# Kernel optimization log

Hardware: AMD Instinct MI355X
Metric: run time of the kernel (lower is better)

## Reference

```python
import jax, jax.numpy as jnp
import numpy as np

T, N, H, L, V, B, MAX_NB = 32, 1024, 256, 128, 800, 256, 15
E = T * N  # total messages; buffer row E is the zero-pad slot


def setup_inputs() -> dict:
    key = jax.random.key(0)
    ks = jax.random.split(key, 12)

    def lin(k, o, i):
        return jax.random.normal(k, (o, i), jnp.float32) / np.float32(np.sqrt(i))

    rng = np.random.default_rng(0)
    # neighbor message indices: at step t only messages produced at steps < t are valid
    h_nei_idx = rng.integers(0, E, size=(T, N, MAX_NB))
    o_nei_idx = rng.integers(0, E, size=(T, N, MAX_NB))
    limit = (np.arange(T) * N)[:, None, None]
    h_nei_idx = np.where(h_nei_idx < limit, h_nei_idx, E)
    o_nei_idx = np.where(o_nei_idx < limit, o_nei_idx, E)

    return dict(
        emb=jax.random.normal(ks[0], (V, H), jnp.float32) * 0.02,
        W_z_w=lin(ks[1], H, 2 * H), W_z_b=jnp.zeros((H,), jnp.float32),
        W_r_w=lin(ks[2], H, H), W_r_b=jnp.zeros((H,), jnp.float32),
        U_r_w=lin(ks[3], H, H),
        W_h_w=lin(ks[4], H, 2 * H), W_h_b=jnp.zeros((H,), jnp.float32),
        W_w=lin(ks[5], H, H + L), W_b=jnp.zeros((H,), jnp.float32),
        Wo_w=lin(ks[6], V, H), Wo_b=jnp.zeros((V,), jnp.float32),
        U_w=lin(ks[7], H, H + L), U_b=jnp.zeros((H,), jnp.float32),
        Ui_w=lin(ks[8], H, 2 * H), Ui_b=jnp.zeros((H,), jnp.float32),
        Uo_w=lin(ks[9], 1, H), Uo_b=jnp.zeros((1,), jnp.float32),
        x_tree_vecs=jax.random.normal(ks[10], (B, L), jnp.float32),
        word_ids=jnp.asarray(rng.integers(0, V, size=(T, N)), jnp.int32),
        h_nei_idx=jnp.asarray(h_nei_idx, jnp.int32),
        o_nei_idx=jnp.asarray(o_nei_idx, jnp.int32),
        contexts=jnp.asarray(rng.integers(0, B, size=(T, N)), jnp.int32),
        pred_targets=jnp.asarray(rng.integers(0, V, size=(T, N)), jnp.int32),
        direction=jnp.asarray(rng.integers(0, 2, size=(T, N)), jnp.int32),
        root_word_ids=jnp.asarray(rng.integers(0, V, size=(B,)), jnp.int32),
        root_o_idx=jnp.asarray(rng.integers(0, E + 1, size=(B, MAX_NB)), jnp.int32),
    )


def reference(emb, W_z_w, W_z_b, W_r_w, W_r_b, U_r_w, W_h_w, W_h_b,
              W_w, W_b, Wo_w, Wo_b, U_w, U_b, Ui_w, Ui_b, Uo_w, Uo_b,
              x_tree_vecs, word_ids, h_nei_idx, o_nei_idx, contexts,
              pred_targets, direction, root_word_ids, root_o_idx):
    f32 = jnp.float32

    def gru(x, h_nei):  # x: [N,H], h_nei: [N,MAX_NB,H]
        sum_h = h_nei.sum(1)
        z = jax.nn.sigmoid(jnp.concatenate([x, sum_h], -1) @ W_z_w.T + W_z_b)
        r = jax.nn.sigmoid((x @ W_r_w.T + W_r_b)[:, None, :] + h_nei @ U_r_w.T)
        gated = (r * h_nei).sum(1)
        h_tilde = jnp.tanh(jnp.concatenate([x, gated], -1) @ W_h_w.T + W_h_b)
        return (1.0 - z) * sum_h + z * h_tilde

    def step(hbuf, xs):
        t, wid, hidx, oidx = xs
        x = emb[wid]                      # [N,H] embedding gather
        new_h = gru(x, hbuf[hidx])        # gather -> GRU
        cur_o = hbuf[oidx].sum(1)         # padded neighbor sum for stop head
        hbuf = jax.lax.dynamic_update_slice(hbuf, new_h, (t * N, 0))  # scatter
        return hbuf, (new_h, jnp.concatenate([x, cur_o], -1))

    hbuf0 = jnp.zeros((E + 1, H), f32)
    hbuf, (new_h_all, stop_h_all) = jax.lax.scan(
        step, hbuf0, (jnp.arange(T), word_ids, h_nei_idx, o_nei_idx))

    def aggregate(hid, ctx, Vw, Vb, Vow, Vob):
        iv = jnp.concatenate([hid, x_tree_vecs[ctx]], -1)
        return jax.nn.relu(iv @ Vw.T + Vb) @ Vow.T + Vob

    # ---- word prediction head: root entries (zero hidden) + direction==1 edges
    pred_hid = jnp.concatenate([jnp.zeros((B, H), f32), new_h_all.reshape(E, H)], 0)
    pred_ctx = jnp.concatenate([jnp.arange(B, dtype=jnp.int32), contexts.reshape(E)], 0)
    pred_tgt = jnp.concatenate([root_word_ids, pred_targets.reshape(E)], 0)
    pred_mask = jnp.concatenate([jnp.ones((B,), f32), direction.reshape(E).astype(f32)], 0)
    scores = aggregate(pred_hid, pred_ctx, W_w, W_b, Wo_w, Wo_b)  # [B+E, V]
    nll = -jnp.take_along_axis(jax.nn.log_softmax(scores, -1), pred_tgt[:, None], 1)[:, 0]
    pred_loss = (nll * pred_mask).sum() / B
    pred_acc = ((scores.argmax(-1) == pred_tgt).astype(f32) * pred_mask).sum() / pred_mask.sum()

    # ---- stop head: all edges + root closing entries
    root_stop = jnp.concatenate([emb[root_word_ids], hbuf[root_o_idx].sum(1)], -1)
    stop_hid = jnp.concatenate([stop_h_all.reshape(E, 2 * H), root_stop], 0)
    stop_ctx = jnp.concatenate([contexts.reshape(E), jnp.arange(B, dtype=jnp.int32)], 0)
    stop_tgt = jnp.concatenate([direction.reshape(E).astype(f32), jnp.zeros((B,), f32)], 0)
    stop_hid = jax.nn.relu(stop_hid @ Ui_w.T + Ui_b)  # U_i with relu
    s = aggregate(stop_hid, stop_ctx, U_w, U_b, Uo_w, Uo_b)[:, 0]
    bce = jnp.maximum(s, 0.0) - s * stop_tgt + jnp.log1p(jnp.exp(-jnp.abs(s)))
    stop_loss = bce.sum() / B
    stop_acc = ((s >= 0.0).astype(f32) == stop_tgt).astype(f32).mean()

    return pred_loss, stop_loss, pred_acc, stop_acc
```

## Files before the change

kernel.cpp:

```cpp
#include <hip/hip_runtime.h>
#include <math.h>


namespace {

constexpr int T_  = 32;
constexpr int N_  = 1024;
constexpr int H_  = 256;
constexpr int NB_ = 15;
constexpr int E_  = T_ * N_;
constexpr int B_  = 256;
constexpr int PREDB_ = (B_ + E_) / 64;
constexpr int STOPB_ = (E_ + B_) / 64;

typedef unsigned short u16;
typedef unsigned int   u32;
typedef unsigned int  uix4  __attribute__((ext_vector_type(4)));
typedef __bf16        bf16x8 __attribute__((ext_vector_type(8)));
typedef float         f32x4  __attribute__((ext_vector_type(4)));

__device__ __forceinline__ float sig_(float x){ return 1.f / (1.f + __expf(-x)); }

__device__ __forceinline__ float b2f(u16 u){
  union { u32 i; float f; } v; v.i = ((u32)u) << 16; return v.f;
}
__device__ __forceinline__ u16 f2b(float f){
  union { float f; u32 i; } v; v.f = f;
  const u32 r = v.i + 0x7fffu + ((v.i >> 16) & 1u);
  return (u16)(r >> 16);
}
__device__ __forceinline__ f32x4 mfma16(uix4 a, uix4 b, f32x4 c){
  return __builtin_amdgcn_mfma_f32_16x16x32_bf16(
      __builtin_bit_cast(bf16x8, a), __builtin_bit_cast(bf16x8, b), c, 0, 0, 0);
}

__global__ __launch_bounds__(256) void k_cvt(
    const float* __restrict__ emb, const float* __restrict__ xt,
    const float* __restrict__ Ww,  const float* __restrict__ Wo,
    const float* __restrict__ Ui,  const float* __restrict__ Uw,
    const float* __restrict__ Wz,  const float* __restrict__ Wr,
    const float* __restrict__ Ur,  const float* __restrict__ Wh,
    u16* __restrict__ o_emb, u16* __restrict__ o_xt, u16* __restrict__ o_Ww,
    u16* __restrict__ o_Wo,  u16* __restrict__ o_Ui, u16* __restrict__ o_Uw,
    u16* __restrict__ o_Wz,  u16* __restrict__ o_Wr, u16* __restrict__ o_Ur,
    u16* __restrict__ o_Wh)
{
  int i = blockIdx.x * 256 + threadIdx.x;
  if (i < 204800){ o_emb[i] = f2b(emb[i]); return; }  i -= 204800;
  if (i <  32768){ o_xt[i]  = f2b(xt[i]);  return; }  i -=  32768;
  if (i <  98304){ o_Ww[i]  = f2b(Ww[i]);  return; }  i -=  98304;
  if (i < 204800){ o_Wo[i]  = f2b(Wo[i]);  return; }  i -= 204800;
  if (i < 131072){ o_Ui[i]  = f2b(Ui[i]);  return; }  i -= 131072;
  if (i <  98304){ o_Uw[i]  = f2b(Uw[i]);  return; }  i -=  98304;
  if (i < 131072){ o_Wz[i]  = f2b(Wz[i]);  return; }  i -= 131072;
  if (i <  65536){ o_Wr[i]  = f2b(Wr[i]);  return; }  i -=  65536;
  if (i <  65536){ o_Ur[i]  = f2b(Ur[i]);  return; }  i -=  65536;
  if (i < 131072){ o_Wh[i]  = f2b(Wh[i]); }
}

__global__ __launch_bounds__(256) void k_rep(
    const u16* __restrict__ Ur16, const u16* __restrict__ Wz16,
    const u16* __restrict__ Wh16,
    u16* __restrict__ UrF, u16* __restrict__ WzF, u16* __restrict__ WhF)
{
  const int idx = blockIdx.x * 256 + threadIdx.x;
  const int mat = idx >> 13, r = idx & 8191;
  const int ctkb = r >> 6, lane = r & 63;
  const int ct = ctkb >> 3, kb = ctkb & 7;
  const int q = lane >> 4, m = lane & 15;
  const int col = ct * 16 + m;
  const u16* src;
  u16* dst;
  if (mat == 0){ src = Ur16 + (size_t)col*256 +       kb*32 + q*8; dst = UrF; }
  else if (mat == 1){ src = Wz16 + (size_t)col*512 + 256 + kb*32 + q*8; dst = WzF; }
  else { src = Wh16 + (size_t)col*512 + 256 + kb*32 + q*8; dst = WhF; }
  *(uix4*)(dst + (size_t)r * 8) = *(const uix4*)src;
}

__global__ __launch_bounds__(256) void k_init(float* __restrict__ acc,
                                              u16* __restrict__ hb16){
  const int tid = threadIdx.x;
  if (tid < 16) acc[tid] = 0.f;
  hb16[(size_t)E_ * H_ + tid] = 0;
}

__global__ __launch_bounds__(256) void k_tab(
    const u16* __restrict__ emb16,
    const u16* __restrict__ Wr16, const float* __restrict__ Wrb,
    const u16* __restrict__ Wz16, const float* __restrict__ Wzb,
    const u16* __restrict__ Wh16, const float* __restrict__ Whb,
    float* __restrict__ xrtab, float* __restrict__ xztab,
    float* __restrict__ xhtab)
{
  const int tid = threadIdx.x;
  const int w = tid >> 6, ln = tid & 63, q = ln >> 4, m = ln & 15;
  const int r0 = blockIdx.x * 16;

  uix4 Ae[8];
  {
    const u16* ep = emb16 + (size_t)(r0 + m) * 256 + q * 8;
    #pragma unroll
    for (int kb = 0; kb < 8; ++kb) Ae[kb] = *(const uix4*)(ep + kb * 32);
  }
  #pragma unroll
  for (int nt = 0; nt < 4; ++nt){
    const int col = w * 64 + nt * 16 + m;
    f32x4 ar = {0.f,0.f,0.f,0.f}, az = {0.f,0.f,0.f,0.f}, ah = {0.f,0.f,0.f,0.f};
    const u16* br = Wr16 + (size_t)col * 256 + q * 8;
    const u16* bz = Wz16 + (size_t)col * 512 + q * 8;
    const u16* bh = Wh16 + (size_t)col * 512 + q * 8;
    #pragma unroll
    for (int kb = 0; kb < 8; ++kb){
      ar = mfma16(Ae[kb], *(const uix4*)(br + kb*32), ar);
      az = mfma16(Ae[kb], *(const uix4*)(bz + kb*32), az);
      ah = mfma16(Ae[kb], *(const uix4*)(bh + kb*32), ah);
    }
    const float rb = Wrb[col], zb = Wzb[col], hb = Whb[col];
    #pragma unroll
    for (int i = 0; i < 4; ++i){
      const size_t o = (size_t)(r0 + 4*q + i) * 256 + col;
      xrtab[o] = ar[i] + rb;
      xztab[o] = az[i] + zb;
      xhtab[o] = ah[i] + hb;
    }
  }
}

__global__ __launch_bounds__(1024, 4) void k_gru(
    const u16* __restrict__ UrF, const u16* __restrict__ WzF,
    const u16* __restrict__ WhF,
    const float* __restrict__ xrtab, const float* __restrict__ xztab,
    const float* __restrict__ xhtab,
    const int* __restrict__ word_ids, const int* __restrict__ h_nei,
    u16* __restrict__ hb16, int t)
{
  __shared__ __align__(16) u16 hn[64 * 264];
  __shared__ __align__(16) u16 sh[4][264];
  __shared__ __align__(16) u16 gl[4][264];
  __shared__ int s_wid[4];
  __shared__ int s_hidx[64];

  const int tid = threadIdx.x;
  const int w = tid >> 6, ln = tid & 63, q = ln >> 4, m = ln & 15;
  const int col  = w * 16 + m;
  const int base = t * N_ + blockIdx.x * 4;

  if (tid < 4) s_wid[tid] = word_ids[base + tid];
  if (tid < 64){
    const int row = tid & 3, nb = tid >> 2;
    s_hidx[tid] = (nb < NB_) ? h_nei[(base + row) * NB_ + nb] : E_;
  }

  const u16* urb = UrF + (size_t)(w * 8) * 512 + ln * 8;
  uix4 b0 = *(const uix4*)(urb);
  uix4 b1 = *(const uix4*)(urb + 512);
  uix4 b2 = *(const uix4*)(urb + 1024);
  uix4 b3 = *(const uix4*)(urb + 1536);
  uix4 b4 = *(const uix4*)(urb + 2048);
  uix4 b5 = *(const uix4*)(urb + 2560);
  uix4 b6 = *(const uix4*)(urb + 3072);
  uix4 b7 = *(const uix4*)(urb + 3584);

  __syncthreads();

  #pragma unroll
  for (int it = 0; it < 2; ++it){
    const int task = it * 1024 + tid;
    const int row = task >> 5, ch = task & 31;
    *(uix4*)(&hn[row*264 + ch*8]) =
        *(const uix4*)(hb16 + (size_t)s_hidx[row]*256 + ch*8);
  }
  __syncthreads();

  f32x4 xr;
  #pragma unroll
  for (int i = 0; i < 4; ++i) xr[i] = xrtab[(size_t)s_wid[i] * 256 + col];

  float ga[4] = {0.f,0.f,0.f,0.f}, su[4] = {0.f,0.f,0.f,0.f};
  #pragma unroll
  for (int j = 0; j < 4; ++j){
    uix4 Ah[8];
    #pragma unroll
    for (int kb = 0; kb < 8; ++kb)
      Ah[kb] = *(const uix4*)(&hn[(j*16 + m)*264 + kb*32 + q*8]);
    f32x4 a = xr;
    a = mfma16(Ah[0], b0, a); a = mfma16(Ah[1], b1, a);
    a = mfma16(Ah[2], b2, a); a = mfma16(Ah[3], b3, a);
    a = mfma16(Ah[4], b4, a); a = mfma16(Ah[5], b5, a);
    a = mfma16(Ah[6], b6, a); a = mfma16(Ah[7], b7, a);
    #pragma unroll
    for (int i = 0; i < 4; ++i){
      const float hv = b2f(hn[(j*16 + 4*q + i)*264 + col]);
      ga[i] += sig_(a[i]) * hv;
      su[i] += hv;
    }
  }

  #pragma unroll
  for (int i = 0; i < 4; ++i){
    ga[i] += __shfl_xor(ga[i], 16, 64);
    ga[i] += __shfl_xor(ga[i], 32, 64);
    su[i] += __shfl_xor(su[i], 16, 64);
    su[i] += __shfl_xor(su[i], 32, 64);
  }
  if (q == 0){
    #pragma unroll
    for (int i = 0; i < 4; ++i){
      sh[i][col] = f2b(su[i]);
      gl[i][col] = f2b(ga[i]);
    }
  }
  __syncthreads();

  f32x4 az, ah;
  #pragma unroll
  for (int i = 0; i < 4; ++i){
    az[i] = xztab[(size_t)s_wid[i] * 256 + col];
    ah[i] = xhtab[(size_t)s_wid[i] * 256 + col];
  }
  {
    const u16* zb = WzF + (size_t)(w * 8) * 512 + ln * 8;
    uix4 Bz[8];
    #pragma unroll
    for (int kb = 0; kb < 8; ++kb) Bz[kb] = *(const uix4*)(zb + kb * 512);
    uix4 As[8];
    #pragma unroll
    for (int kb = 0; kb < 8; ++kb) As[kb] = *(const uix4*)(&sh[m & 3][kb*32 + q*8]);
    #pragma unroll
    for (int kb = 0; kb < 8; ++kb) az = mfma16(As[kb], Bz[kb], az);
  }
  {
    const u16* hb = WhF + (size_t)(w * 8) * 512 + ln * 8;
    uix4 Bh[8];
    #pragma unroll
    for (int kb = 0; kb < 8; ++kb) Bh[kb] = *(const uix4*)(hb + kb * 512);
    uix4 Ag[8];
    #pragma unroll
    for (int kb = 0; kb < 8; ++kb) Ag[kb] = *(const uix4*)(&gl[m & 3][kb*32 + q*8]);
    #pragma unroll
    for (int kb = 0; kb < 8; ++kb) ah = mfma16(Ag[kb], Bh[kb], ah);
  }
  if (q == 0){
    #pragma unroll
    for (int i = 0; i < 4; ++i){
      const float z  = sig_(az[i]);
      const float ht = tanhf(ah[i]);
      const float nh = (1.f - z) * su[i] + z * ht;
      hb16[(size_t)(base + i) * 256 + col] = f2b(nh);
    }
  }
}

struct PredSm {
  u16   hd[4][16][264];
  u16   bt[16][392];
  int   tgt[64];
  float mask[64];
  float nll[64], hit[64], msk[64];
};
struct StopSm {
  u16   so[64][264];
  u16   bt[16][392];
  int   oidx[64][NB_];
  int   wid[64], ctx[64];
  float tgt[64];
  float b0[64], b1[64];
};
constexpr size_t SMU_ = sizeof(StopSm) > sizeof(PredSm) ? sizeof(StopSm)
                                                        : sizeof(PredSm);

__device__ void pred_body(int bid, char* smraw,
    const u16* __restrict__ hb16, const u16* __restrict__ Ww16,
    const float* __restrict__ Wb, const u16* __restrict__ Wo16,
    const float* __restrict__ Wob, const u16* __restrict__ xt16,
    const int* __restrict__ contexts, const int* __restrict__ pred_targets,
    const int* __restrict__ direction, const int* __restrict__ root_word_ids,
    float* __restrict__ accum)
{
  PredSm& sm = *(PredSm*)smraw;
  const int tid = threadIdx.x;
  const int p0  = bid * 64;
  const int w = tid >> 6, ln = tid & 63, q = ln >> 4, m = ln & 15;
  const int r0 = w * 16;

  if (tid < 64){
    const int p = p0 + tid;
    int tg; float mk;
    if (p < B_){ tg = root_word_ids[p]; mk = 1.f; }
    else { tg = pred_targets[p - B_]; mk = (float)direction[p - B_]; }
    sm.tgt[tid] = tg; sm.mask[tid] = mk;
  }
  const int p    = p0 + r0 + m;
  const int hrow = (p < B_) ? E_ : (p - B_);
  const int ctx  = (p < B_) ? p  : contexts[p - B_];

  uix4 A1[12];
  {
    const u16* hp = hb16 + (size_t)hrow * 256 + q * 8;
    #pragma unroll
    for (int j = 0; j < 8; ++j) A1[j] = *(const uix4*)(hp + j * 32);
    const u16* xp = xt16 + (size_t)ctx * 128 + q * 8;
    #pragma unroll
    for (int j = 0; j < 4; ++j) A1[8 + j] = *(const uix4*)(xp + j * 32);
  }

  {
    #pragma unroll
    for (int j = 0; j < 3; ++j){
      const int i = j*256 + tid, r = i / 48, c = i % 48;
      *(uix4*)(&sm.bt[r][c*8]) = *(const uix4*)(Ww16 + (size_t)i*8);
    }
  }
  __syncthreads();
  for (int t = 0; t < 16; ++t){
    uix4 pf[3];
    if (t < 15){
      const u16* src = Ww16 + (size_t)(t+1)*16*384;
      #pragma unroll
      for (int j = 0; j < 3; ++j)
        pf[j] = *(const uix4*)(src + (size_t)(j*256 + tid)*8);
    }
    f32x4 acc = {0.f, 0.f, 0.f, 0.f};
    const u16* bp = &sm.bt[m][q*8];
    #pragma unroll
    for (int j = 0; j < 12; ++j) acc = mfma16(A1[j], *(const uix4*)(bp + j*32), acc);
    const float bias = Wb[t*16 + m];
    #pragma unroll
    for (int i = 0; i < 4; ++i)
      sm.hd[w][q*4 + i][t*16 + m] = f2b(fmaxf(acc[i] + bias, 0.f));
    __syncthreads();
    if (t < 15){
      #pragma unroll
      for (int j = 0; j < 3; ++j){
        const int i = j*256 + tid, r = i / 48, c = i % 48;
        *(uix4*)(&sm.bt[r][c*8]) = pf[j];
      }
      __syncthreads();
    }
  }

  uix4 A2[8];
  #pragma unroll
  for (int j = 0; j < 8; ++j) A2[j] = *(const uix4*)(&sm.hd[w][m][j*32 + q*8]);

  int tgtc[4];
  #pragma unroll
  for (int i = 0; i < 4; ++i) tgtc[i] = sm.tgt[r0 + q*4 + i];
  float lrun[4], amax[4], tval[4]; int aidx[4];
  #pragma unroll
  for (int i = 0; i < 4; ++i){
    lrun[i] = 0.f; amax[i] = -1e30f; tval[i] = -1e30f; aidx[i] = 0;
  }

  {
    #pragma unroll
    for (int j = 0; j < 2; ++j){
      const int i = j*256 + tid, r = i >> 5, c = i & 31;
      *(uix4*)(&sm.bt[r][c*8]) = *(const uix4*)(Wo16 + (size_t)i*8);
    }
  }
  __syncthreads();
  for (int t = 0; t < 50; ++t){
    uix4 pf[2];
    if (t < 49){
      const u16* src = Wo16 + (size_t)(t+1)*16*256;
      #pragma unroll
      for (int j = 0; j < 2; ++j)
        pf[j] = *(const uix4*)(src + (size_t)(j*256 + tid)*8);
    }
    f32x4 acc = {0.f, 0.f, 0.f, 0.f};
    const u16* bp = &sm.bt[m][q*8];
    #pragma unroll
    for (int j = 0; j < 8; ++j) acc = mfma16(A2[j], *(const uix4*)(bp + j*32), acc);
    const int c = t*16 + m;
    const float bias = Wob[c];
    #pragma unroll
    for (int i = 0; i < 4; ++i){
      const float v = acc[i] + bias;
      if (c == tgtc[i]) tval[i] = v;
      if (v > amax[i]){ amax[i] = v; aidx[i] = c; }
      lrun[i] += __expf(v);
    }
    __syncthreads();
    if (t < 49){
      #pragma unroll
      for (int j = 0; j < 2; ++j){
        const int i = j*256 + tid, r = i >> 5, cc = i & 31;
        *(uix4*)(&sm.bt[r][cc*8]) = pf[j];
      }
      __syncthreads();
    }
  }
  #pragma unroll
  for (int msk = 1; msk < 16; msk <<= 1){
    #pragma unroll
    for (int i = 0; i < 4; ++i){
      lrun[i] += __shfl_xor(lrun[i], msk, 64);
      const float oa = __shfl_xor(amax[i], msk, 64);
      const int   oi = __shfl_xor(aidx[i], msk, 64);
      if (oa > amax[i] || (oa == amax[i] && oi < aidx[i])){ amax[i] = oa; aidx[i] = oi; }
      tval[i] = fmaxf(tval[i], __shfl_xor(tval[i], msk, 64));
    }
  }
  if (m == 0){
    #pragma unroll
    for (int i = 0; i < 4; ++i){
      const int r = r0 + q*4 + i;
      const float mk  = sm.mask[r];
      const float nll = __logf(lrun[i]) - tval[i];
      sm.nll[r] = nll * mk;
      sm.hit[r] = (aidx[i] == tgtc[i]) ? mk : 0.f;
      sm.msk[r] = mk;
    }
  }
  __syncthreads();
  if (tid < 64){
    float a = sm.nll[tid], b = sm.hit[tid], c2 = sm.msk[tid];
    #pragma unroll
    for (int off = 32; off > 0; off >>= 1){
      a += __shfl_down(a, off, 64); b += __shfl_down(b, off, 64); c2 += __shfl_down(c2, off, 64);
    }
    if (tid == 0){
      atomicAdd(&accum[0], a); atomicAdd(&accum[1], b); atomicAdd(&accum[2], c2);
    }
  }
}

__device__ void stop_body(int bid, char* smraw,
    const u16* __restrict__ hb16, const u16* __restrict__ emb16,
    const u16* __restrict__ Ui16, const float* __restrict__ Uib,
    const u16* __restrict__ Uw16, const float* __restrict__ Ub,
    const float* __restrict__ Uo, const float* __restrict__ Uob,
    const u16* __restrict__ xt16,
    const int* __restrict__ word_ids, const int* __restrict__ o_nei,
    const int* __restrict__ contexts, const int* __restrict__ direction,
    const int* __restrict__ root_word_ids, const int* __restrict__ root_o_idx,
    float* __restrict__ accum)
{
  StopSm& sm = *(StopSm*)smraw;
  const int tid = threadIdx.x;
  const int p0  = bid * 64;
  const int w = tid >> 6, ln = tid & 63, q = ln >> 4, m = ln & 15;
  const int r0 = w * 16;

  if (tid < 64){
    const int s = p0 + tid;
    if (s < E_){ sm.wid[tid] = word_ids[s]; sm.ctx[tid] = contexts[s];
                 sm.tgt[tid] = (float)direction[s]; }
    else { const int b = s - E_; sm.wid[tid] = root_word_ids[b]; sm.ctx[tid] = b;
           sm.tgt[tid] = 0.f; }
  }
  for (int k = tid; k < 64 * NB_; k += 256){
    const int r = k / NB_, nb = k % NB_;
    const int s = p0 + r;
    sm.oidx[r][nb] = (s < E_) ? o_nei[(size_t)s * NB_ + nb]
                              : root_o_idx[(size_t)(s - E_) * NB_ + nb];
  }
  __syncthreads();

  for (int it = 0; it < 4; ++it){
    const int task = it * 256 + tid;
    const int row = task >> 4, sl = task & 15;
    float a[16];
    #pragma unroll
    for (int c = 0; c < 16; ++c) a[c] = 0.f;
    #pragma unroll
    for (int nb = 0; nb < NB_; ++nb){
      const u16* p = hb16 + (size_t)sm.oidx[row][nb] * 256 + sl * 16;
      const uix4 v0 = *(const uix4*)(p);
      const uix4 v1 = *(const uix4*)(p + 8);
      #pragma unroll
      for (int c = 0; c < 4; ++c){
        a[2*c]     += b2f((u16)(v0[c] & 0xffffu));
        a[2*c + 1] += b2f((u16)(v0[c] >> 16));
        a[8 + 2*c] += b2f((u16)(v1[c] & 0xffffu));
        a[9 + 2*c] += b2f((u16)(v1[c] >> 16));
      }
    }
    uix4 o0, o1;
    #pragma unroll
    for (int c = 0; c < 4; ++c){
      o0[c] = (u32)f2b(a[2*c])   | ((u32)f2b(a[2*c+1]) << 16);
      o1[c] = (u32)f2b(a[8+2*c]) | ((u32)f2b(a[9+2*c]) << 16);
    }
    *(uix4*)(&sm.so[row][sl*16])     = o0;
    *(uix4*)(&sm.so[row][sl*16 + 8]) = o1;
  }
  __syncthreads();

  uix4 A1[16];
  {
    const u16* ep = emb16 + (size_t)sm.wid[r0 + m] * 256 + q * 8;
    #pragma unroll
    for (int j = 0; j < 8; ++j) A1[j] = *(const uix4*)(ep + j * 32);
    #pragma unroll
    for (int j = 0; j < 8; ++j) A1[8 + j] = *(const uix4*)(&sm.so[r0 + m][j*32 + q*8]);
  }
  __syncthreads();

  for (int t = 0; t < 16; ++t){
    f32x4 acc = {0.f, 0.f, 0.f, 0.f};
    const u16* bp = Ui16 + (size_t)(t*16 + m) * 512 + q * 8;
    #pragma unroll
    for (int j = 0; j < 16; ++j) acc = mfma16(A1[j], *(const uix4*)(bp + j*32), acc);
    const float bias = Uib[t*16 + m];
    #pragma unroll
    for (int i = 0; i < 4; ++i)
      sm.so[r0 + q*4 + i][t*16 + m] = f2b(fmaxf(acc[i] + bias, 0.f));
  }
  __syncthreads();

  uix4 A2[12];
  {
    #pragma unroll
    for (int j = 0; j < 8; ++j) A2[j] = *(const uix4*)(&sm.so[r0 + m][j*32 + q*8]);
    const u16* xp = xt16 + (size_t)sm.ctx[r0 + m] * 128 + q * 8;
    #pragma unroll
    for (int j = 0; j < 4; ++j) A2[8 + j] = *(const uix4*)(xp + j * 32);
  }
  float sp[4] = {0.f, 0.f, 0.f, 0.f};
  {
    #pragma unroll
    for (int j = 0; j < 3; ++j){
      const int i = j*256 + tid, r = i / 48, c = i % 48;
      *(uix4*)(&sm.bt[r][c*8]) = *(const uix4*)(Uw16 + (size_t)i*8);
    }
  }
  __syncthreads();
  for (int t = 0; t < 16; ++t){
    uix4 pf[3];
    if (t < 15){
      const u16* src = Uw16 + (size_t)(t+1)*16*384;
      #pragma unroll
      for (int j = 0; j < 3; ++j)
        pf[j] = *(const uix4*)(src + (size_t)(j*256 + tid)*8);
    }
    f32x4 acc = {0.f, 0.f, 0.f, 0.f};
    const u16* bp = &sm.bt[m][q*8];
    #pragma unroll
    for (int j = 0; j < 12; ++j) acc = mfma16(A2[j], *(const uix4*)(bp + j*32), acc);
    const int c = t*16 + m;
    const float bias = Ub[c];
    const float uo   = Uo[c];
    #pragma unroll
    for (int i = 0; i < 4; ++i) sp[i] += fmaxf(acc[i] + bias, 0.f) * uo;
    __syncthreads();
    if (t < 15){
      #pragma unroll
      for (int j = 0; j < 3; ++j){
        const int i = j*256 + tid, r = i / 48, cc = i % 48;
        *(uix4*)(&sm.bt[r][cc*8]) = pf[j];
      }
      __syncthreads();
    }
  }
  #pragma unroll
  for (int msk = 1; msk < 16; msk <<= 1){
    #pragma unroll
    for (int i = 0; i < 4; ++i) sp[i] += __shfl_xor(sp[i], msk, 64);
  }
  if (m == 0){
    const float ub = Uob[0];
    #pragma unroll
    for (int i = 0; i < 4; ++i){
      const int r = r0 + q*4 + i;
      const float s   = sp[i] + ub;
      const float tgt = sm.tgt[r];
      sm.b0[r] = fmaxf(s, 0.f) - s * tgt + log1pf(__expf(-fabsf(s)));
      const float pb = (s >= 0.f) ? 1.f : 0.f;
      sm.b1[r] = (pb == tgt) ? 1.f : 0.f;
    }
  }
  __syncthreads();
  if (tid < 64){
    float a = sm.b0[tid], b = sm.b1[tid];
    #pragma unroll
    for (int off = 32; off > 0; off >>= 1){
      a += __shfl_down(a, off, 64); b += __shfl_down(b, off, 64);
    }
    if (tid == 0){ atomicAdd(&accum[3], a); atomicAdd(&accum[4], b); }
  }
}

__global__ __launch_bounds__(256, 3) void k_heads(
    const u16* __restrict__ hb16, const u16* __restrict__ emb16,
    const u16* __restrict__ Ww16, const float* __restrict__ Wb,
    const u16* __restrict__ Wo16, const float* __restrict__ Wob,
    const u16* __restrict__ Ui16, const float* __restrict__ Uib,
    const u16* __restrict__ Uw16, const float* __restrict__ Ub,
    const float* __restrict__ Uo, const float* __restrict__ Uob,
    const u16* __restrict__ xt16,
    const int* __restrict__ word_ids, const int* __restrict__ o_nei,
    const int* __restrict__ contexts, const int* __restrict__ pred_targets,
    const int* __restrict__ direction, const int* __restrict__ root_word_ids,
    const int* __restrict__ root_o_idx, float* __restrict__ accum)
{
  __shared__ __align__(16) char smraw[SMU_];
  const int b = blockIdx.x;
  if (b < PREDB_){
    pred_body(b, smraw, hb16, Ww16, Wb, Wo16, Wob, xt16,
              contexts, pred_targets, direction, root_word_ids, accum);
  } else {
    stop_body(b - PREDB_, smraw, hb16, emb16, Ui16, Uib, Uw16, Ub, Uo, Uob,
              xt16, word_ids, o_nei, contexts, direction,
              root_word_ids, root_o_idx, accum);
  }
}

__global__ void k_final(const float* __restrict__ acc, float* __restrict__ out){
  if (threadIdx.x == 0 && blockIdx.x == 0){
    out[0] = acc[0] / (float)B_;
    out[1] = acc[3] / (float)B_;
    out[2] = acc[1] / acc[2];
    out[3] = acc[4] / (float)(E_ + B_);
  }
}

}

extern "C" void kernel_launch(void* const* d_in, const int* in_sizes, int n_in,
                              void* d_out, int out_size, void* d_ws, size_t ws_size,
                              hipStream_t stream)
{
  const float* emb   = (const float*)d_in[0];
  const float* Wz    = (const float*)d_in[1];
  const float* Wzb   = (const float*)d_in[2];
  const float* Wr    = (const float*)d_in[3];
  const float* Wrb   = (const float*)d_in[4];
  const float* Ur    = (const float*)d_in[5];
  const float* Wh    = (const float*)d_in[6];
  const float* Whb   = (const float*)d_in[7];
  const float* Ww    = (const float*)d_in[8];
  const float* Wb    = (const float*)d_in[9];
  const float* Wo    = (const float*)d_in[10];
  const float* Wob   = (const float*)d_in[11];
  const float* Uw    = (const float*)d_in[12];
  const float* Ub    = (const float*)d_in[13];
  const float* Ui    = (const float*)d_in[14];
  const float* Uib   = (const float*)d_in[15];
  const float* Uo    = (const float*)d_in[16];
  const float* Uob   = (const float*)d_in[17];
  const float* xtree = (const float*)d_in[18];
  const int* word_ids      = (const int*)d_in[19];
  const int* h_nei_idx     = (const int*)d_in[20];
  const int* o_nei_idx     = (const int*)d_in[21];
  const int* contexts      = (const int*)d_in[22];
  const int* pred_targets  = (const int*)d_in[23];
  const int* direction     = (const int*)d_in[24];
  const int* root_word_ids = (const int*)d_in[25];
  const int* root_o_idx    = (const int*)d_in[26];

  char*  wsb   = (char*)d_ws;
  float* accum = (float*)wsb;
  size_t off = 256 + 4096;
  u16* hb16  = (u16*)(wsb + off); off += (size_t)(E_ + 1) * H_ * 2;
  u16* emb16 = (u16*)(wsb + off); off += 204800u * 2;
  u16* xt16  = (u16*)(wsb + off); off += 32768u * 2;
  u16* Ww16  = (u16*)(wsb + off); off += 98304u * 2;
  u16* Wo16  = (u16*)(wsb + off); off += 204800u * 2;
  u16* Ui16  = (u16*)(wsb + off); off += 131072u * 2;
  u16* Uw16  = (u16*)(wsb + off); off += 98304u * 2;
  u16* Wz16  = (u16*)(wsb + off); off += 131072u * 2;
  u16* Wr16  = (u16*)(wsb + off); off += 65536u * 2;
  u16* Ur16  = (u16*)(wsb + off); off += 65536u * 2;
  u16* Wh16  = (u16*)(wsb + off); off += 131072u * 2;
  u16* UrF   = (u16*)(wsb + off); off += 65536u * 2;
  u16* WzF   = (u16*)(wsb + off); off += 65536u * 2;
  u16* WhF   = (u16*)(wsb + off); off += 65536u * 2;
  float* xrtab = (float*)(wsb + off); off += 204800u * 4;
  float* xztab = (float*)(wsb + off); off += 204800u * 4;
  float* xhtab = (float*)(wsb + off); off += 204800u * 4;
  float* out = (float*)d_out;

  hipLaunchKernelGGL(k_cvt, dim3(4544), dim3(256), 0, stream,
                     emb, xtree, Ww, Wo, Ui, Uw, Wz, Wr, Ur, Wh,
                     emb16, xt16, Ww16, Wo16, Ui16, Uw16,
                     Wz16, Wr16, Ur16, Wh16);
  hipLaunchKernelGGL(k_init, dim3(1), dim3(256), 0, stream, accum, hb16);
  hipLaunchKernelGGL(k_rep, dim3(96), dim3(256), 0, stream,
                     Ur16, Wz16, Wh16, UrF, WzF, WhF);
  hipLaunchKernelGGL(k_tab, dim3(50), dim3(256), 0, stream,
                     emb16, Wr16, Wrb, Wz16, Wzb, Wh16, Whb,
                     xrtab, xztab, xhtab);

  for (int t = 0; t < T_; ++t){
    hipLaunchKernelGGL(k_gru, dim3(N_ / 4), dim3(1024), 0, stream,
                       UrF, WzF, WhF, xrtab, xztab, xhtab,
                       word_ids, h_nei_idx, hb16, t);
  }

  hipLaunchKernelGGL(k_heads, dim3(PREDB_ + STOPB_), dim3(256), 0, stream,
                     hb16, emb16, Ww16, Wb, Wo16, Wob, Ui16, Uib, Uw16, Ub,
                     Uo, Uob, xt16, word_ids, o_nei_idx, contexts,
                     pred_targets, direction, root_word_ids, root_o_idx,
                     accum);

  hipLaunchKernelGGL(k_final, dim3(1), dim3(1), 0, stream, accum, out);
}
```

Before: 624.8 us.

## Process one GRU row per 256-thread block instead of four rows per block

The per-step GRU kernel now launches N blocks of 256 threads, each handling a single message row, instead of N/4 blocks of 1024 threads handling four rows. Each wave covers 64 output columns across four column tiles and streams the Ur, Wz and Wh fragments from global memory inside the loop rather than keeping them in registers. The aim is smaller blocks with cheaper barriers and a smaller shared-memory footprint, so more blocks can be scheduled per step. The cost is that every block re-reads the full weight matrices, which is four times the weight traffic per row. The z and h matmuls also fill only one of 16 MFMA rows, which wastes more matrix-core work than before.

```diff
diff --git a/kernel.cpp b/kernel.cpp
--- a/kernel.cpp
+++ b/kernel.cpp
@@ -126,7 +126,7 @@
   }
 }
 
-__global__ __launch_bounds__(1024, 4) void k_gru(
+__global__ __launch_bounds__(256, 4) void k_gru(
     const u16* __restrict__ UrF, const u16* __restrict__ WzF,
     const u16* __restrict__ WhF,
     const float* __restrict__ xrtab, const float* __restrict__ xztab,
@@ -134,119 +134,87 @@
     const int* __restrict__ word_ids, const int* __restrict__ h_nei,
     u16* __restrict__ hb16, int t)
 {
-  __shared__ __align__(16) u16 hn[64 * 264];
-  __shared__ __align__(16) u16 sh[4][264];
-  __shared__ __align__(16) u16 gl[4][264];
-  __shared__ int s_wid[4];
-  __shared__ int s_hidx[64];
+  __shared__ __align__(16) u16 hn[16 * 264];
+  __shared__ __align__(16) u16 sh[264];
+  __shared__ __align__(16) u16 gl[264];
+  __shared__ int s_hidx[16];
 
   const int tid = threadIdx.x;
   const int w = tid >> 6, ln = tid & 63, q = ln >> 4, m = ln & 15;
-  const int col  = w * 16 + m;
-  const int base = t * N_ + blockIdx.x * 4;
-
-  if (tid < 4) s_wid[tid] = word_ids[base + tid];
-  if (tid < 64){
-    const int row = tid & 3, nb = tid >> 2;
-    s_hidx[tid] = (nb < NB_) ? h_nei[(base + row) * NB_ + nb] : E_;
-  }
-
-  const u16* urb = UrF + (size_t)(w * 8) * 512 + ln * 8;
-  uix4 b0 = *(const uix4*)(urb);
-  uix4 b1 = *(const uix4*)(urb + 512);
-  uix4 b2 = *(const uix4*)(urb + 1024);
-  uix4 b3 = *(const uix4*)(urb + 1536);
-  uix4 b4 = *(const uix4*)(urb + 2048);
-  uix4 b5 = *(const uix4*)(urb + 2560);
-  uix4 b6 = *(const uix4*)(urb + 3072);
-  uix4 b7 = *(const uix4*)(urb + 3584);
-
+  const int row = t * N_ + blockIdx.x;
+
+  if (tid < 16)
+    s_hidx[tid] = (tid < NB_) ? h_nei[row * NB_ + tid] : E_;
+  const int wid = word_ids[row];
   __syncthreads();
 
   #pragma unroll
   for (int it = 0; it < 2; ++it){
-    const int task = it * 1024 + tid;
-    const int row = task >> 5, ch = task & 31;
-    *(uix4*)(&hn[row*264 + ch*8]) =
-        *(const uix4*)(hb16 + (size_t)s_hidx[row]*256 + ch*8);
-  }
-  __syncthreads();
-
-  f32x4 xr;
-  #pragma unroll
-  for (int i = 0; i < 4; ++i) xr[i] = xrtab[(size_t)s_wid[i] * 256 + col];
-
-  float ga[4] = {0.f,0.f,0.f,0.f}, su[4] = {0.f,0.f,0.f,0.f};
-  #pragma unroll
-  for (int j = 0; j < 4; ++j){
-    uix4 Ah[8];
-    #pragma unroll
-    for (int kb = 0; kb < 8; ++kb)
-      Ah[kb] = *(const uix4*)(&hn[(j*16 + m)*264 + kb*32 + q*8]);
-    f32x4 a = xr;
-    a = mfma16(Ah[0], b0, a); a = mfma16(Ah[1], b1, a);
-    a = mfma16(Ah[2], b2, a); a = mfma16(Ah[3], b3, a);
-    a = mfma16(Ah[4], b4, a); a = mfma16(Ah[5], b5, a);
-    a = mfma16(Ah[6], b6, a); a = mfma16(Ah[7], b7, a);
+    const int task = it * 256 + tid;
+    const int r = task >> 5, ch = task & 31;
+    *(uix4*)(&hn[r*264 + ch*8]) =
+        *(const uix4*)(hb16 + (size_t)s_hidx[r]*256 + ch*8);
+  }
+  __syncthreads();
+
+  uix4 Ah[8];
+  #pragma unroll
+  for (int kb = 0; kb < 8; ++kb)
+    Ah[kb] = *(const uix4*)(&hn[m*264 + kb*32 + q*8]);
+
+  float ga[4], su[4];
+  #pragma unroll
+  for (int ct = 0; ct < 4; ++ct){
+    const int col = w*64 + ct*16 + m;
+    const float xr = xrtab[(size_t)wid * 256 + col];
+    f32x4 a = {xr, xr, xr, xr};
+    const u16* bp = UrF + (size_t)((w*4 + ct)*8) * 512 + ln * 8;
+    #pragma unroll
+    for (int kb = 0; kb < 8; ++kb) a = mfma16(Ah[kb], *(const uix4*)(bp + kb*512), a);
+    float pg = 0.f, ps = 0.f;
     #pragma unroll
     for (int i = 0; i < 4; ++i){
-      const float hv = b2f(hn[(j*16 + 4*q + i)*264 + col]);
-      ga[i] += sig_(a[i]) * hv;
-      su[i] += hv;
-    }
-  }
-
-  #pragma unroll
-  for (int i = 0; i < 4; ++i){
-    ga[i] += __shfl_xor(ga[i], 16, 64);
-    ga[i] += __shfl_xor(ga[i], 32, 64);
-    su[i] += __shfl_xor(su[i], 16, 64);
-    su[i] += __shfl_xor(su[i], 32, 64);
+      const float hv = b2f(hn[(4*q + i)*264 + col]);
+      pg += sig_(a[i]) * hv;
+      ps += hv;
+    }
+    pg += __shfl_xor(pg, 16, 64); pg += __shfl_xor(pg, 32, 64);
+    ps += __shfl_xor(ps, 16, 64); ps += __shfl_xor(ps, 32, 64);
+    ga[ct] = pg; su[ct] = ps;
   }
   if (q == 0){
     #pragma unroll
-    for (int i = 0; i < 4; ++i){
-      sh[i][col] = f2b(su[i]);
-      gl[i][col] = f2b(ga[i]);
-    }
-  }
-  __syncthreads();
-
-  f32x4 az, ah;
-  #pragma unroll
-  for (int i = 0; i < 4; ++i){
-    az[i] = xztab[(size_t)s_wid[i] * 256 + col];
-    ah[i] = xhtab[(size_t)s_wid[i] * 256 + col];
-  }
-  {
-    const u16* zb = WzF + (size_t)(w * 8) * 512 + ln * 8;
-    uix4 Bz[8];
-    #pragma unroll
-    for (int kb = 0; kb < 8; ++kb) Bz[kb] = *(const uix4*)(zb + kb * 512);
-    uix4 As[8];
-    #pragma unroll
-    for (int kb = 0; kb < 8; ++kb) As[kb] = *(const uix4*)(&sh[m & 3][kb*32 + q*8]);
-    #pragma unroll
-    for (int kb = 0; kb < 8; ++kb) az = mfma16(As[kb], Bz[kb], az);
-  }
-  {
-    const u16* hb = WhF + (size_t)(w * 8) * 512 + ln * 8;
-    uix4 Bh[8];
-    #pragma unroll
-    for (int kb = 0; kb < 8; ++kb) Bh[kb] = *(const uix4*)(hb + kb * 512);
-    uix4 Ag[8];
-    #pragma unroll
-    for (int kb = 0; kb < 8; ++kb) Ag[kb] = *(const uix4*)(&gl[m & 3][kb*32 + q*8]);
-    #pragma unroll
-    for (int kb = 0; kb < 8; ++kb) ah = mfma16(Ag[kb], Bh[kb], ah);
-  }
-  if (q == 0){
-    #pragma unroll
-    for (int i = 0; i < 4; ++i){
-      const float z  = sig_(az[i]);
-      const float ht = tanhf(ah[i]);
-      const float nh = (1.f - z) * su[i] + z * ht;
-      hb16[(size_t)(base + i) * 256 + col] = f2b(nh);
+    for (int ct = 0; ct < 4; ++ct){
+      sh[w*64 + ct*16 + m] = f2b(su[ct]);
+      gl[w*64 + ct*16 + m] = f2b(ga[ct]);
+    }
+  }
+  __syncthreads();
+
+  uix4 As[8], Ag[8];
+  #pragma unroll
+  for (int kb = 0; kb < 8; ++kb){
+    As[kb] = *(const uix4*)(&sh[kb*32 + q*8]);
+    Ag[kb] = *(const uix4*)(&gl[kb*32 + q*8]);
+  }
+  #pragma unroll
+  for (int ct = 0; ct < 4; ++ct){
+    const int col = w*64 + ct*16 + m;
+    const float xz = xztab[(size_t)wid * 256 + col];
+    const float xh = xhtab[(size_t)wid * 256 + col];
+    f32x4 az = {xz, xz, xz, xz};
+    f32x4 ah = {xh, xh, xh, xh};
+    const u16* zb = WzF + (size_t)((w*4 + ct)*8) * 512 + ln * 8;
+    const u16* hb = WhF + (size_t)((w*4 + ct)*8) * 512 + ln * 8;
+    #pragma unroll
+    for (int kb = 0; kb < 8; ++kb) az = mfma16(As[kb], *(const uix4*)(zb + kb*512), az);
+    #pragma unroll
+    for (int kb = 0; kb < 8; ++kb) ah = mfma16(Ag[kb], *(const uix4*)(hb + kb*512), ah);
+    if (q == 0){
+      const float z  = sig_(az[0]);
+      const float ht = tanhf(ah[0]);
+      const float nh = (1.f - z) * su[ct] + z * ht;
+      hb16[(size_t)row * 256 + col] = f2b(nh);
     }
   }
 }
@@ -684,7 +652,7 @@
                      xrtab, xztab, xhtab);
 
   for (int t = 0; t < T_; ++t){
-    hipLaunchKernelGGL(k_gru, dim3(N_ / 4), dim3(1024), 0, stream,
+    hipLaunchKernelGGL(k_gru, dim3(N_), dim3(256), 0, stream,
                        UrF, WzF, WhF, xrtab, xztab, xhtab,
                        word_ids, h_nei_idx, hb16, t);
   }
```

Result: slower. 799.7 us (+28.0%).

## Pre-swizzle Ui weights into fragment layout and widen Wo tiles to 32 columns

Applied to the files above, without the earlier changes.

Adds a repack of the Ui weight matrix into MFMA fragment order so the stop head loads it with coalesced contiguous 16-byte reads and batches all 16 B fragments before the MFMAs. The prediction head's Wo loop now processes 32 output columns per iteration with two accumulators, halving the barrier and staging count per block. This costs a larger shared-memory tile, more registers, and an extra repack pass.

```diff
diff --git a/kernel.cpp b/kernel.cpp
--- a/kernel.cpp
+++ b/kernel.cpp
@@ -60,21 +60,33 @@
 
 __global__ __launch_bounds__(256) void k_rep(
     const u16* __restrict__ Ur16, const u16* __restrict__ Wz16,
-    const u16* __restrict__ Wh16,
-    u16* __restrict__ UrF, u16* __restrict__ WzF, u16* __restrict__ WhF)
+    const u16* __restrict__ Wh16, const u16* __restrict__ Ui16,
+    u16* __restrict__ UrF, u16* __restrict__ WzF, u16* __restrict__ WhF,
+    u16* __restrict__ UiF)
 {
   const int idx = blockIdx.x * 256 + threadIdx.x;
-  const int mat = idx >> 13, r = idx & 8191;
-  const int ctkb = r >> 6, lane = r & 63;
-  const int ct = ctkb >> 3, kb = ctkb & 7;
-  const int q = lane >> 4, m = lane & 15;
-  const int col = ct * 16 + m;
-  const u16* src;
-  u16* dst;
-  if (mat == 0){ src = Ur16 + (size_t)col*256 +       kb*32 + q*8; dst = UrF; }
-  else if (mat == 1){ src = Wz16 + (size_t)col*512 + 256 + kb*32 + q*8; dst = WzF; }
-  else { src = Wh16 + (size_t)col*512 + 256 + kb*32 + q*8; dst = WhF; }
-  *(uix4*)(dst + (size_t)r * 8) = *(const uix4*)src;
+  if (idx < 24576){
+    const int mat = idx >> 13, r = idx & 8191;
+    const int ctkb = r >> 6, lane = r & 63;
+    const int ct = ctkb >> 3, kb = ctkb & 7;
+    const int q = lane >> 4, m = lane & 15;
+    const int col = ct * 16 + m;
+    const u16* src;
+    u16* dst;
+    if (mat == 0){ src = Ur16 + (size_t)col*256 +       kb*32 + q*8; dst = UrF; }
+    else if (mat == 1){ src = Wz16 + (size_t)col*512 + 256 + kb*32 + q*8; dst = WzF; }
+    else { src = Wh16 + (size_t)col*512 + 256 + kb*32 + q*8; dst = WhF; }
+    *(uix4*)(dst + (size_t)r * 8) = *(const uix4*)src;
+  } else {
+    const int r = idx - 24576;
+    if (r >= 16384) return;
+    const int ctkb = r >> 6, lane = r & 63;
+    const int ct = ctkb >> 4, kb = ctkb & 15;
+    const int q = lane >> 4, m = lane & 15;
+    const int col = ct * 16 + m;
+    *(uix4*)(UiF + (size_t)r * 8) =
+        *(const uix4*)(Ui16 + (size_t)col*512 + kb*32 + q*8);
+  }
 }
 
 __global__ __launch_bounds__(256) void k_init(float* __restrict__ acc,
@@ -253,14 +265,14 @@
 
 struct PredSm {
   u16   hd[4][16][264];
-  u16   bt[16][392];
+  u16   bt[32 * 264];
   int   tgt[64];
   float mask[64];
   float nll[64], hit[64], msk[64];
 };
 struct StopSm {
   u16   so[64][264];
-  u16   bt[16][392];
+  u16   bt[16 * 392];
   int   oidx[64][NB_];
   int   wid[64], ctx[64];
   float tgt[64];
@@ -308,7 +320,7 @@
     #pragma unroll
     for (int j = 0; j < 3; ++j){
       const int i = j*256 + tid, r = i / 48, c = i % 48;
-      *(uix4*)(&sm.bt[r][c*8]) = *(const uix4*)(Ww16 + (size_t)i*8);
+      *(uix4*)(&sm.bt[r*392 + c*8]) = *(const uix4*)(Ww16 + (size_t)i*8);
     }
   }
   __syncthreads();
@@ -321,7 +333,7 @@
         pf[j] = *(const uix4*)(src + (size_t)(j*256 + tid)*8);
     }
     f32x4 acc = {0.f, 0.f, 0.f, 0.f};
-    const u16* bp = &sm.bt[m][q*8];
+    const u16* bp = &sm.bt[m*392 + q*8];
     #pragma unroll
     for (int j = 0; j < 12; ++j) acc = mfma16(A1[j], *(const uix4*)(bp + j*32), acc);
     const float bias = Wb[t*16 + m];
@@ -333,7 +345,7 @@
       #pragma unroll
       for (int j = 0; j < 3; ++j){
         const int i = j*256 + tid, r = i / 48, c = i % 48;
-        *(uix4*)(&sm.bt[r][c*8]) = pf[j];
+        *(uix4*)(&sm.bt[r*392 + c*8]) = pf[j];
       }
       __syncthreads();
     }
@@ -354,39 +366,46 @@
 
   {
     #pragma unroll
-    for (int j = 0; j < 2; ++j){
+    for (int j = 0; j < 4; ++j){
       const int i = j*256 + tid, r = i >> 5, c = i & 31;
-      *(uix4*)(&sm.bt[r][c*8]) = *(const uix4*)(Wo16 + (size_t)i*8);
-    }
-  }
-  __syncthreads();
-  for (int t = 0; t < 50; ++t){
-    uix4 pf[2];
-    if (t < 49){
-      const u16* src = Wo16 + (size_t)(t+1)*16*256;
+      *(uix4*)(&sm.bt[r*264 + c*8]) = *(const uix4*)(Wo16 + (size_t)i*8);
+    }
+  }
+  __syncthreads();
+  for (int pp = 0; pp < 25; ++pp){
+    uix4 pf[4];
+    if (pp < 24){
+      const u16* src = Wo16 + (size_t)(pp+1)*32*256;
       #pragma unroll
-      for (int j = 0; j < 2; ++j)
+      for (int j = 0; j < 4; ++j)
         pf[j] = *(const uix4*)(src + (size_t)(j*256 + tid)*8);
     }
-    f32x4 acc = {0.f, 0.f, 0.f, 0.f};
-    const u16* bp = &sm.bt[m][q*8];
-    #pragma unroll
-    for (int j = 0; j < 8; ++j) acc = mfma16(A2[j], *(const uix4*)(bp + j*32), acc);
-    const int c = t*16 + m;
-    const float bias = Wob[c];
+    f32x4 a0 = {0.f,0.f,0.f,0.f}, a1 = {0.f,0.f,0.f,0.f};
+    const u16* bp0 = &sm.bt[m*264 + q*8];
+    const u16* bp1 = &sm.bt[(16 + m)*264 + q*8];
+    #pragma unroll
+    for (int j = 0; j < 8; ++j){
+      a0 = mfma16(A2[j], *(const uix4*)(bp0 + j*32), a0);
+      a1 = mfma16(A2[j], *(const uix4*)(bp1 + j*32), a1);
+    }
+    const int c0 = pp*32 + m, c1 = c0 + 16;
+    const float bias0 = Wob[c0], bias1 = Wob[c1];
     #pragma unroll
     for (int i = 0; i < 4; ++i){
-      const float v = acc[i] + bias;
-      if (c == tgtc[i]) tval[i] = v;
-      if (v > amax[i]){ amax[i] = v; aidx[i] = c; }
-      lrun[i] += __expf(v);
+      const float v0 = a0[i] + bias0;
+      const float v1 = a1[i] + bias1;
+      if (c0 == tgtc[i]) tval[i] = v0;
+      if (c1 == tgtc[i]) tval[i] = v1;
+      if (v0 > amax[i]){ amax[i] = v0; aidx[i] = c0; }
+      if (v1 > amax[i]){ amax[i] = v1; aidx[i] = c1; }
+      lrun[i] += __expf(v0) + __expf(v1);
     }
     __syncthreads();
-    if (t < 49){
+    if (pp < 24){
       #pragma unroll
-      for (int j = 0; j < 2; ++j){
+      for (int j = 0; j < 4; ++j){
         const int i = j*256 + tid, r = i >> 5, cc = i & 31;
-        *(uix4*)(&sm.bt[r][cc*8]) = pf[j];
+        *(uix4*)(&sm.bt[r*264 + cc*8]) = pf[j];
       }
       __syncthreads();
     }
@@ -428,7 +447,7 @@
 
 __device__ void stop_body(int bid, char* smraw,
     const u16* __restrict__ hb16, const u16* __restrict__ emb16,
-    const u16* __restrict__ Ui16, const float* __restrict__ Uib,
+    const u16* __restrict__ UiF,  const float* __restrict__ Uib,
     const u16* __restrict__ Uw16, const float* __restrict__ Ub,
     const float* __restrict__ Uo, const float* __restrict__ Uob,
     const u16* __restrict__ xt16,
@@ -499,10 +518,13 @@
   __syncthreads();
 
   for (int t = 0; t < 16; ++t){
+    const u16* bp = UiF + (size_t)(t * 16) * 512 + ln * 8;
+    uix4 Bf[16];
+    #pragma unroll
+    for (int kb = 0; kb < 16; ++kb) Bf[kb] = *(const uix4*)(bp + kb * 512);
     f32x4 acc = {0.f, 0.f, 0.f, 0.f};
-    const u16* bp = Ui16 + (size_t)(t*16 + m) * 512 + q * 8;
-    #pragma unroll
-    for (int j = 0; j < 16; ++j) acc = mfma16(A1[j], *(const uix4*)(bp + j*32), acc);
+    #pragma unroll
+    for (int kb = 0; kb < 16; ++kb) acc = mfma16(A1[kb], Bf[kb], acc);
     const float bias = Uib[t*16 + m];
     #pragma unroll
     for (int i = 0; i < 4; ++i)
@@ -523,7 +545,7 @@
     #pragma unroll
     for (int j = 0; j < 3; ++j){
       const int i = j*256 + tid, r = i / 48, c = i % 48;
-      *(uix4*)(&sm.bt[r][c*8]) = *(const uix4*)(Uw16 + (size_t)i*8);
+      *(uix4*)(&sm.bt[r*392 + c*8]) = *(const uix4*)(Uw16 + (size_t)i*8);
     }
   }
   __syncthreads();
@@ -536,7 +558,7 @@
         pf[j] = *(const uix4*)(src + (size_t)(j*256 + tid)*8);
     }
     f32x4 acc = {0.f, 0.f, 0.f, 0.f};
-    const u16* bp = &sm.bt[m][q*8];
+    const u16* bp = &sm.bt[m*392 + q*8];
     #pragma unroll
     for (int j = 0; j < 12; ++j) acc = mfma16(A2[j], *(const uix4*)(bp + j*32), acc);
     const int c = t*16 + m;
@@ -549,7 +571,7 @@
       #pragma unroll
       for (int j = 0; j < 3; ++j){
         const int i = j*256 + tid, r = i / 48, cc = i % 48;
-        *(uix4*)(&sm.bt[r][cc*8]) = pf[j];
+        *(uix4*)(&sm.bt[r*392 + cc*8]) = pf[j];
       }
       __syncthreads();
     }
@@ -586,7 +608,7 @@
     const u16* __restrict__ hb16, const u16* __restrict__ emb16,
     const u16* __restrict__ Ww16, const float* __restrict__ Wb,
     const u16* __restrict__ Wo16, const float* __restrict__ Wob,
-    const u16* __restrict__ Ui16, const float* __restrict__ Uib,
+    const u16* __restrict__ UiF,  const float* __restrict__ Uib,
     const u16* __restrict__ Uw16, const float* __restrict__ Ub,
     const float* __restrict__ Uo, const float* __restrict__ Uob,
     const u16* __restrict__ xt16,
@@ -601,7 +623,7 @@
     pred_body(b, smraw, hb16, Ww16, Wb, Wo16, Wob, xt16,
               contexts, pred_targets, direction, root_word_ids, accum);
   } else {
-    stop_body(b - PREDB_, smraw, hb16, emb16, Ui16, Uib, Uw16, Ub, Uo, Uob,
+    stop_body(b - PREDB_, smraw, hb16, emb16, UiF, Uib, Uw16, Ub, Uo, Uob,
               xt16, word_ids, o_nei, contexts, direction,
               root_word_ids, root_o_idx, accum);
   }
@@ -667,6 +689,7 @@
   u16* UrF   = (u16*)(wsb + off); off += 65536u * 2;
   u16* WzF   = (u16*)(wsb + off); off += 65536u * 2;
   u16* WhF   = (u16*)(wsb + off); off += 65536u * 2;
+  u16* UiF   = (u16*)(wsb + off); off += 131072u * 2;
   float* xrtab = (float*)(wsb + off); off += 204800u * 4;
   float* xztab = (float*)(wsb + off); off += 204800u * 4;
   float* xhtab = (float*)(wsb + off); off += 204800u * 4;
@@ -677,8 +700,8 @@
                      emb16, xt16, Ww16, Wo16, Ui16, Uw16,
                      Wz16, Wr16, Ur16, Wh16);
   hipLaunchKernelGGL(k_init, dim3(1), dim3(256), 0, stream, accum, hb16);
-  hipLaunchKernelGGL(k_rep, dim3(96), dim3(256), 0, stream,
-                     Ur16, Wz16, Wh16, UrF, WzF, WhF);
+  hipLaunchKernelGGL(k_rep, dim3(160), dim3(256), 0, stream,
+                     Ur16, Wz16, Wh16, Ui16, UrF, WzF, WhF, UiF);
   hipLaunchKernelGGL(k_tab, dim3(50), dim3(256), 0, stream,
                      emb16, Wr16, Wrb, Wz16, Wzb, Wh16, Whb,
                      xrtab, xztab, xhtab);
@@ -690,7 +713,7 @@
   }
 
   hipLaunchKernelGGL(k_heads, dim3(PREDB_ + STOPB_), dim3(256), 0, stream,
-                     hb16, emb16, Ww16, Wb, Wo16, Wob, Ui16, Uib, Uw16, Ub,
+                     hb16, emb16, Ww16, Wb, Wo16, Wob, UiF, Uib, Uw16, Ub,
                      Uo, Uob, xt16, word_ids, o_nei_idx, contexts,
                      pred_targets, direction, root_word_ids, root_o_idx,
                      accum);
```

After: 578.8 us. 1.08x faster.
